# Performance work log

Measured on AMD Instinct MI355X. Metric: run time of the kernel, lower is better.

Reference implementation:

```python
import jax, jax.numpy as jnp
import numpy as np

B, T, A, IN = 128, 512, 2, 192
N_SESS, RDIM, OUT = 512, 64, 256


def setup_inputs() -> dict:
    key = jax.random.key(0)
    k1, k2, k3, k4 = jax.random.split(key, 4)
    state_in = jax.random.normal(k1, (B, T, A, IN), dtype=jnp.float32)
    session = jax.random.randint(k2, (B,), 0, N_SESS, dtype=jnp.int64)
    # kaiming-uniform-like init scale, exact distribution irrelevant for correctness baseline
    unique_readin = jax.random.normal(k3, (N_SESS, IN, RDIM), dtype=jnp.float32) * (1.0 / np.sqrt(IN))
    project = jax.random.normal(k4, (RDIM, OUT), dtype=jnp.float32) * (1.0 / np.sqrt(RDIM))
    return {"state_in": state_in, "session": session,
            "unique_readin": unique_readin, "project": project}


def reference(state_in, session, unique_readin, project):
    # gather per-sample readin matrices: [B, IN, RDIM]
    readin_matrix = unique_readin[session]
    # btai,bih->btah : per-sample matmul over the input-feature axis
    h = jnp.einsum('btai,bih->btah', state_in, readin_matrix)
    # low-rank compression projection to model dim: [B, T, A, OUT]
    out = jnp.matmul(h, project)
    return out
```

## Files before the change

### kernel.cpp

```cpp
#include <hip/hip_runtime.h>
#include <hip/hip_bf16.h>
#include <stdint.h>


typedef short    bf16x8 __attribute__((ext_vector_type(8)));
typedef float    f32x4  __attribute__((ext_vector_type(4)));
typedef uint32_t u32x2  __attribute__((ext_vector_type(2)));
typedef uint32_t u32x4  __attribute__((ext_vector_type(4)));

#define NB    128
#define MPB   1024
#define INF   192
#define RDIM  64
#define OUTF  256

#define WAIT_VM4()   asm volatile("s_waitcnt vmcnt(4)" ::: "memory")
#define WAIT_VM0()   asm volatile("s_waitcnt vmcnt(0)" ::: "memory")
#define WAIT_LGKM0() asm volatile("s_waitcnt lgkmcnt(0)" ::: "memory")

__device__ __forceinline__ uint16_t f2bf(float f) {
    union { float f; uint32_t u; } v; v.f = f;
    return (uint16_t)((v.u + 0x7fffu + ((v.u >> 16) & 1u)) >> 16);
}
__device__ __forceinline__ uint32_t pack2(float a, float b) {
    return (uint32_t)f2bf(a) | ((uint32_t)f2bf(b) << 16);
}
__device__ __forceinline__ bf16x8 cvt8(f32x4 a, f32x4 b) {
    union { __hip_bfloat162 h2[4]; bf16x8 h; } r;
    r.h2[0] = __float22bfloat162_rn({a[0], a[1]});
    r.h2[1] = __float22bfloat162_rn({a[2], a[3]});
    r.h2[2] = __float22bfloat162_rn({b[0], b[1]});
    r.h2[3] = __float22bfloat162_rn({b[2], b[3]});
    return r.h;
}
__device__ __forceinline__ void gl_lds16(const void* g, void* l) {
    auto gp = (const __attribute__((address_space(1))) uint32_t*)(uintptr_t)g;
    auto lp = (__attribute__((address_space(3))) uint32_t*)(uintptr_t)l;
    __builtin_amdgcn_global_load_lds(gp, lp, 16, 0, 0);
}

__global__ __launch_bounds__(256, 2) void fused_gemm(
    const float* __restrict__ X,
    const int*   __restrict__ session,
    const float* __restrict__ readin,
    const float* __restrict__ project,
    float*       __restrict__ Y)
{
    __shared__ __attribute__((aligned(16))) uint8_t arena[81920];

    const int bid0 = blockIdx.x;
    const int bid  = ((bid0 & 7) << 7) | (bid0 >> 3);
    const int b  = bid >> 3;
    const int mt = (bid >> 1) & 3;
    const int nt = bid & 1;
    const int t  = threadIdx.x, l = t & 63, w = t >> 6;
    const int lr = l & 15, lk = l >> 4;

    const float* Xb = X + ((size_t)b * MPB + mt * 256) * INF;
    float*       Yb = Y + ((size_t)b * MPB + mt * 256) * OUTF + nt * 128;

    uint8_t* Ab = arena + 49152 + w * 8192;
    int asrc[4];
#pragma unroll
    for (int c = 0; c < 4; ++c) {
        int i   = c * 64 + l;
        int row = i >> 3;
        int kq  = (i & 7) ^ (row & 7);
        asrc[c] = row * INF + kq * 4;
    }
    const float* Aw = Xb + (size_t)(w * 32) * INF;

    auto stage = [&](int s, int buf) {
        const float* src = Aw + (s / 6) * (128 * INF) + (s % 6) * 32;
#pragma unroll
        for (int c = 0; c < 4; ++c)
            gl_lds16(src + asrc[c], Ab + buf * 4096 + c * 1024);
    };

    stage(0, 0);
    stage(1, 1);

    {
        uint16_t* Rl = (uint16_t*)arena;
        uint16_t* Pl = (uint16_t*)(arena + 24576);
        const float* Rg = readin + (size_t)session[b] * (INF * RDIM);

#pragma unroll
        for (int c = 0; c < 3; ++c) {
            int idx = c * 4096 + t * 16;
            int row = idx >> 6;
            int kg0 = (idx & 63) >> 3;
            f32x4 v0 = *(const f32x4*)(Rg + idx);
            f32x4 v1 = *(const f32x4*)(Rg + idx + 4);
            f32x4 v2 = *(const f32x4*)(Rg + idx + 8);
            f32x4 v3 = *(const f32x4*)(Rg + idx + 12);
            u32x4 d0, d1;
            d0[0] = pack2(v0[0], v0[1]); d0[1] = pack2(v0[2], v0[3]);
            d0[2] = pack2(v1[0], v1[1]); d0[3] = pack2(v1[2], v1[3]);
            d1[0] = pack2(v2[0], v2[1]); d1[1] = pack2(v2[2], v2[3]);
            d1[2] = pack2(v3[0], v3[1]); d1[3] = pack2(v3[2], v3[3]);
            *(u32x4*)&Rl[row * 64 + (((kg0    ) ^ (row & 7)) << 3)] = d0;
            *(u32x4*)&Rl[row * 64 + (((kg0 + 1) ^ (row & 7)) << 3)] = d1;
        }
        {
            int h  = t >> 2;
            int og = (t & 3) * 32;
            const float* Pg = project + (size_t)h * OUTF + nt * 128 + og;
#pragma unroll
            for (int q = 0; q < 8; ++q) {
                f32x4 v = *(const f32x4*)(Pg + q * 4);
#pragma unroll
                for (int e = 0; e < 4; ++e) {
                    int o = og + q * 4 + e;
                    Pl[o * 64 + (((h >> 3) ^ (o & 7)) << 3) + (h & 7)] = f2bf(v[e]);
                }
            }
        }
        __syncthreads();

        const int wm = w >> 1, wn = w & 1;
        f32x4 wacc[6][4];
#pragma unroll
        for (int n = 0; n < 6; ++n)
#pragma unroll
            for (int m = 0; m < 4; ++m) wacc[n][m] = f32x4{0.f, 0.f, 0.f, 0.f};

#pragma unroll
        for (int kk = 0; kk < 2; ++kk) {
            int kg = kk * 4 + lk;
            bf16x8 a[4], bb[6];
#pragma unroll
            for (int m = 0; m < 4; ++m) {
                int row = wm * 64 + m * 16 + lr;
                a[m] = *(const bf16x8*)&Pl[row * 64 + ((kg ^ (row & 7)) << 3)];
            }
#pragma unroll
            for (int n = 0; n < 6; ++n) {
                int col = wn * 96 + n * 16 + lr;
                bb[n] = *(const bf16x8*)&Rl[col * 64 + ((kg ^ (col & 7)) << 3)];
            }
#pragma unroll
            for (int n = 0; n < 6; ++n)
#pragma unroll
                for (int m = 0; m < 4; ++m)
                    wacc[n][m] = __builtin_amdgcn_mfma_f32_16x16x32_bf16(
                        bb[n], a[m], wacc[n][m], 0, 0, 0);
        }
        __syncthreads();

        uint16_t* Bs16 = (uint16_t*)arena;
#pragma unroll
        for (int n = 0; n < 6; ++n) {
            int ubase = (wn * 12 + n * 2 + (lk >> 1)) * 128;
#pragma unroll
            for (int m = 0; m < 4; ++m) {
                int o = wm * 64 + m * 16 + lr;
                u32x2 d;
                d[0] = pack2(wacc[n][m][0], wacc[n][m][1]);
                d[1] = pack2(wacc[n][m][2], wacc[n][m][3]);
                *(u32x2*)&Bs16[(size_t)(ubase + o) * 8 + (lk & 1) * 4] = d;
            }
        }
        __syncthreads();
    }

    f32x4 accA[2][8], accB[2][8];
#pragma unroll
    for (int m = 0; m < 2; ++m)
#pragma unroll
        for (int n = 0; n < 8; ++n) {
            accA[m][n] = f32x4{0.f, 0.f, 0.f, 0.f};
            accB[m][n] = f32x4{0.f, 0.f, 0.f, 0.f};
        }

    const int a0s = ((2 * lk)     ^ (lr & 7)) << 4;
    const int a1s = ((2 * lk + 1) ^ (lr & 7)) << 4;

#pragma unroll
    for (int s = 0; s < 12; ++s) {
        if (s < 10) { WAIT_VM4(); } else { WAIT_VM0(); }
        __builtin_amdgcn_sched_barrier(0);

        const uint8_t* Abuf = Ab + (s & 1) * 4096;
        const int kk = s % 6;
        bf16x8 af[2], bfr[8];
#pragma unroll
        for (int m = 0; m < 2; ++m) {
            const uint8_t* p = Abuf + (m * 16 + lr) * 128;
            f32x4 lo = *(const f32x4*)(p + a0s);
            f32x4 hi = *(const f32x4*)(p + a1s);
            af[m] = cvt8(lo, hi);
        }
#pragma unroll
        for (int n = 0; n < 8; ++n)
            bfr[n] = *(const bf16x8*)(arena
                        + (((kk * 4 + lk) * 128 + n * 16 + lr) << 4));

        WAIT_LGKM0();
        __builtin_amdgcn_sched_barrier(0);
        if (s < 10) stage(s + 2, s & 1);

        if (s < 6) {
#pragma unroll
            for (int m = 0; m < 2; ++m)
#pragma unroll
                for (int n = 0; n < 8; ++n)
                    accA[m][n] = __builtin_amdgcn_mfma_f32_16x16x32_bf16(
                        af[m], bfr[n], accA[m][n], 0, 0, 0);
        } else {
#pragma unroll
            for (int m = 0; m < 2; ++m)
#pragma unroll
                for (int n = 0; n < 8; ++n)
                    accB[m][n] = __builtin_amdgcn_mfma_f32_16x16x32_bf16(
                        af[m], bfr[n], accB[m][n], 0, 0, 0);
        }
    }

#pragma unroll
    for (int m = 0; m < 2; ++m) {
        int r0 = w * 32 + m * 16 + lk * 4;
#pragma unroll
        for (int n = 0; n < 8; ++n) {
            int c0 = n * 16 + lr;
#pragma unroll
            for (int j = 0; j < 4; ++j) {
                Yb[(size_t)(r0 + j) * OUTF + c0]       = accA[m][n][j];
                Yb[(size_t)(128 + r0 + j) * OUTF + c0] = accB[m][n][j];
            }
        }
    }
}

extern "C" void kernel_launch(void* const* d_in, const int* in_sizes, int n_in,
                              void* d_out, int out_size, void* d_ws, size_t ws_size,
                              hipStream_t stream) {
    (void)in_sizes; (void)n_in; (void)out_size; (void)d_ws; (void)ws_size;
    const float* state   = (const float*)d_in[0];
    const int*   session = (const int*)  d_in[1];
    const float* readin  = (const float*)d_in[2];
    const float* project = (const float*)d_in[3];
    float*       out     = (float*)d_out;

    hipLaunchKernelGGL(fused_gemm, dim3(1024), dim3(256), 0, stream,
                       state, session, readin, project, out);
}
```

Baseline: 45.33 us.

## Double rows per block and stream output stores per 128-row chunk

Each block now covers 512 rows instead of 256, and the grid shrinks to 512 blocks, so the per-sample fused weight matrix (readin times project, built in bf16) is computed half as often. A single accumulator set is reused across four 128-row chunks. Each chunk's result is written as vectorized f32x4 stores inside the K loop, using swapped MFMA operands so each lane's values are contiguous along the output row. Wait counts are relaxed to let those stores overlap later loads. The risk is lower occupancy and parallelism (512 blocks over the device's CUs) and a more fragile vmcnt accounting.

```diff
diff --git a/kernel.cpp b/kernel.cpp
--- a/kernel.cpp
+++ b/kernel.cpp
@@ -14,6 +14,7 @@
 #define RDIM  64
 #define OUTF  256
 
+#define WAIT_VM20()  asm volatile("s_waitcnt vmcnt(20)" ::: "memory")
 #define WAIT_VM4()   asm volatile("s_waitcnt vmcnt(4)" ::: "memory")
 #define WAIT_VM0()   asm volatile("s_waitcnt vmcnt(0)" ::: "memory")
 #define WAIT_LGKM0() asm volatile("s_waitcnt lgkmcnt(0)" ::: "memory")
@@ -49,15 +50,15 @@
     __shared__ __attribute__((aligned(16))) uint8_t arena[81920];
 
     const int bid0 = blockIdx.x;
-    const int bid  = ((bid0 & 7) << 7) | (bid0 >> 3);
-    const int b  = bid >> 3;
-    const int mt = (bid >> 1) & 3;
+    const int bid  = ((bid0 & 7) << 6) | (bid0 >> 3);
+    const int b  = bid >> 2;
+    const int mt = (bid >> 1) & 1;
     const int nt = bid & 1;
     const int t  = threadIdx.x, l = t & 63, w = t >> 6;
     const int lr = l & 15, lk = l >> 4;
 
-    const float* Xb = X + ((size_t)b * MPB + mt * 256) * INF;
-    float*       Yb = Y + ((size_t)b * MPB + mt * 256) * OUTF + nt * 128;
+    const float* Xb = X + ((size_t)b * MPB + mt * 512) * INF;
+    float*       Yb = Y + ((size_t)b * MPB + mt * 512) * OUTF + nt * 128;
 
     uint8_t* Ab = arena + 49152 + w * 8192;
     int asrc[4];
@@ -164,25 +165,26 @@
         __syncthreads();
     }
 
-    f32x4 accA[2][8], accB[2][8];
+    f32x4 acc[2][8];
 #pragma unroll
     for (int m = 0; m < 2; ++m)
 #pragma unroll
-        for (int n = 0; n < 8; ++n) {
-            accA[m][n] = f32x4{0.f, 0.f, 0.f, 0.f};
-            accB[m][n] = f32x4{0.f, 0.f, 0.f, 0.f};
-        }
+        for (int n = 0; n < 8; ++n) acc[m][n] = f32x4{0.f, 0.f, 0.f, 0.f};
 
     const int a0s = ((2 * lk)     ^ (lr & 7)) << 4;
     const int a1s = ((2 * lk + 1) ^ (lr & 7)) << 4;
 
 #pragma unroll
-    for (int s = 0; s < 12; ++s) {
-        if (s < 10) { WAIT_VM4(); } else { WAIT_VM0(); }
+    for (int s = 0; s < 24; ++s) {
+        const int h  = s / 6;
+        const int kk = s % 6;
+
+        if (s == 23)                    { WAIT_VM0(); }
+        else if (s >= 6 && kk < 2)      { WAIT_VM20(); }
+        else                            { WAIT_VM4(); }
         __builtin_amdgcn_sched_barrier(0);
 
         const uint8_t* Abuf = Ab + (s & 1) * 4096;
-        const int kk = s % 6;
         bf16x8 af[2], bfr[8];
 #pragma unroll
         for (int m = 0; m < 2; ++m) {
@@ -198,35 +200,30 @@
 
         WAIT_LGKM0();
         __builtin_amdgcn_sched_barrier(0);
-        if (s < 10) stage(s + 2, s & 1);
-
-        if (s < 6) {
-#pragma unroll
-            for (int m = 0; m < 2; ++m)
+        if (s < 22) stage(s + 2, s & 1);
+
+#pragma unroll
+        for (int m = 0; m < 2; ++m)
+#pragma unroll
+            for (int n = 0; n < 8; ++n)
+                acc[m][n] = __builtin_amdgcn_mfma_f32_16x16x32_bf16(
+                    bfr[n], af[m], acc[m][n], 0, 0, 0);
+
+        if (kk == 5) {
+#pragma unroll
+            for (int m = 0; m < 2; ++m) {
+                float* yr = Yb + (size_t)(h * 128 + w * 32 + m * 16 + lr) * OUTF
+                          + lk * 4;
 #pragma unroll
                 for (int n = 0; n < 8; ++n)
-                    accA[m][n] = __builtin_amdgcn_mfma_f32_16x16x32_bf16(
-                        af[m], bfr[n], accA[m][n], 0, 0, 0);
-        } else {
-#pragma unroll
-            for (int m = 0; m < 2; ++m)
-#pragma unroll
-                for (int n = 0; n < 8; ++n)
-                    accB[m][n] = __builtin_amdgcn_mfma_f32_16x16x32_bf16(
-                        af[m], bfr[n], accB[m][n], 0, 0, 0);
-        }
-    }
-
-#pragma unroll
-    for (int m = 0; m < 2; ++m) {
-        int r0 = w * 32 + m * 16 + lk * 4;
-#pragma unroll
-        for (int n = 0; n < 8; ++n) {
-            int c0 = n * 16 + lr;
-#pragma unroll
-            for (int j = 0; j < 4; ++j) {
-                Yb[(size_t)(r0 + j) * OUTF + c0]       = accA[m][n][j];
-                Yb[(size_t)(128 + r0 + j) * OUTF + c0] = accB[m][n][j];
+                    *(f32x4*)(yr + n * 16) = acc[m][n];
+            }
+            if (s != 23) {
+#pragma unroll
+                for (int m = 0; m < 2; ++m)
+#pragma unroll
+                    for (int n = 0; n < 8; ++n)
+                        acc[m][n] = f32x4{0.f, 0.f, 0.f, 0.f};
             }
         }
     }
@@ -242,6 +239,6 @@
     const float* project = (const float*)d_in[3];
     float*       out     = (float*)d_out;
 
-    hipLaunchKernelGGL(fused_gemm, dim3(1024), dim3(256), 0, stream,
+    hipLaunchKernelGGL(fused_gemm, dim3(512), dim3(256), 0, stream,
                        state, session, readin, project, out);
 }
```

After: 47.24 us. +4.2%, slower.

## Use 512-thread blocks, halve per-wave tile, and store outputs mid-loop with swapped MFMA operands

Applied to the files above, without the earlier changes.

Doubles the threads per block to eight waves, so each wave handles 16 rows instead of 32. This halves the per-wave A staging, the readin/project conversion work and the weight-fusion MFMA tile. The main loop swaps the MFMA operand order so each lane holds four contiguous output columns. It writes results as 16-byte vector stores right after each half finishes, instead of scalar stores at the end, and adjusts the vmcnt waits for the overlapping store traffic. This aims to cut register pressure and uncoalesced scalar stores and to raise latency hiding, at the risk of lower occupancy with 512-thread blocks and the 80 KB LDS arena.

```diff
diff --git a/kernel.cpp b/kernel.cpp
--- a/kernel.cpp
+++ b/kernel.cpp
@@ -14,7 +14,8 @@
 #define RDIM  64
 #define OUTF  256
 
-#define WAIT_VM4()   asm volatile("s_waitcnt vmcnt(4)" ::: "memory")
+#define WAIT_VM10()  asm volatile("s_waitcnt vmcnt(10)" ::: "memory")
+#define WAIT_VM2()   asm volatile("s_waitcnt vmcnt(2)" ::: "memory")
 #define WAIT_VM0()   asm volatile("s_waitcnt vmcnt(0)" ::: "memory")
 #define WAIT_LGKM0() asm volatile("s_waitcnt lgkmcnt(0)" ::: "memory")
 
@@ -39,7 +40,7 @@
     __builtin_amdgcn_global_load_lds(gp, lp, 16, 0, 0);
 }
 
-__global__ __launch_bounds__(256, 2) void fused_gemm(
+__global__ __launch_bounds__(512, 2) void fused_gemm(
     const float* __restrict__ X,
     const int*   __restrict__ session,
     const float* __restrict__ readin,
@@ -59,22 +60,22 @@
     const float* Xb = X + ((size_t)b * MPB + mt * 256) * INF;
     float*       Yb = Y + ((size_t)b * MPB + mt * 256) * OUTF + nt * 128;
 
-    uint8_t* Ab = arena + 49152 + w * 8192;
-    int asrc[4];
-#pragma unroll
-    for (int c = 0; c < 4; ++c) {
+    uint8_t* Ab = arena + 49152 + w * 4096;
+    int asrc[2];
+#pragma unroll
+    for (int c = 0; c < 2; ++c) {
         int i   = c * 64 + l;
         int row = i >> 3;
         int kq  = (i & 7) ^ (row & 7);
         asrc[c] = row * INF + kq * 4;
     }
-    const float* Aw = Xb + (size_t)(w * 32) * INF;
+    const float* Aw = Xb + (size_t)(w * 16) * INF;
 
     auto stage = [&](int s, int buf) {
         const float* src = Aw + (s / 6) * (128 * INF) + (s % 6) * 32;
 #pragma unroll
-        for (int c = 0; c < 4; ++c)
-            gl_lds16(src + asrc[c], Ab + buf * 4096 + c * 1024);
+        for (int c = 0; c < 2; ++c)
+            gl_lds16(src + asrc[c], Ab + buf * 2048 + c * 1024);
     };
 
     stage(0, 0);
@@ -87,27 +88,22 @@
 
 #pragma unroll
         for (int c = 0; c < 3; ++c) {
-            int idx = c * 4096 + t * 16;
+            int idx = c * 4096 + t * 8;
             int row = idx >> 6;
-            int kg0 = (idx & 63) >> 3;
+            int kg0 = t & 7;
             f32x4 v0 = *(const f32x4*)(Rg + idx);
             f32x4 v1 = *(const f32x4*)(Rg + idx + 4);
-            f32x4 v2 = *(const f32x4*)(Rg + idx + 8);
-            f32x4 v3 = *(const f32x4*)(Rg + idx + 12);
-            u32x4 d0, d1;
+            u32x4 d0;
             d0[0] = pack2(v0[0], v0[1]); d0[1] = pack2(v0[2], v0[3]);
             d0[2] = pack2(v1[0], v1[1]); d0[3] = pack2(v1[2], v1[3]);
-            d1[0] = pack2(v2[0], v2[1]); d1[1] = pack2(v2[2], v2[3]);
-            d1[2] = pack2(v3[0], v3[1]); d1[3] = pack2(v3[2], v3[3]);
-            *(u32x4*)&Rl[row * 64 + (((kg0    ) ^ (row & 7)) << 3)] = d0;
-            *(u32x4*)&Rl[row * 64 + (((kg0 + 1) ^ (row & 7)) << 3)] = d1;
+            *(u32x4*)&Rl[row * 64 + ((kg0 ^ (row & 7)) << 3)] = d0;
         }
         {
-            int h  = t >> 2;
-            int og = (t & 3) * 32;
+            int h  = t >> 3;
+            int og = (t & 7) * 16;
             const float* Pg = project + (size_t)h * OUTF + nt * 128 + og;
 #pragma unroll
-            for (int q = 0; q < 8; ++q) {
+            for (int q = 0; q < 4; ++q) {
                 f32x4 v = *(const f32x4*)(Pg + q * 4);
 #pragma unroll
                 for (int e = 0; e < 4; ++e) {
@@ -118,29 +114,29 @@
         }
         __syncthreads();
 
-        const int wm = w >> 1, wn = w & 1;
-        f32x4 wacc[6][4];
-#pragma unroll
-        for (int n = 0; n < 6; ++n)
+        const int wn = w & 3, wm = w >> 2;
+        f32x4 wacc[3][4];
+#pragma unroll
+        for (int n = 0; n < 3; ++n)
 #pragma unroll
             for (int m = 0; m < 4; ++m) wacc[n][m] = f32x4{0.f, 0.f, 0.f, 0.f};
 
 #pragma unroll
         for (int kk = 0; kk < 2; ++kk) {
             int kg = kk * 4 + lk;
-            bf16x8 a[4], bb[6];
+            bf16x8 a[4], bb[3];
 #pragma unroll
             for (int m = 0; m < 4; ++m) {
                 int row = wm * 64 + m * 16 + lr;
                 a[m] = *(const bf16x8*)&Pl[row * 64 + ((kg ^ (row & 7)) << 3)];
             }
 #pragma unroll
-            for (int n = 0; n < 6; ++n) {
-                int col = wn * 96 + n * 16 + lr;
+            for (int n = 0; n < 3; ++n) {
+                int col = wn * 48 + n * 16 + lr;
                 bb[n] = *(const bf16x8*)&Rl[col * 64 + ((kg ^ (col & 7)) << 3)];
             }
 #pragma unroll
-            for (int n = 0; n < 6; ++n)
+            for (int n = 0; n < 3; ++n)
 #pragma unroll
                 for (int m = 0; m < 4; ++m)
                     wacc[n][m] = __builtin_amdgcn_mfma_f32_16x16x32_bf16(
@@ -150,8 +146,8 @@
 
         uint16_t* Bs16 = (uint16_t*)arena;
 #pragma unroll
-        for (int n = 0; n < 6; ++n) {
-            int ubase = (wn * 12 + n * 2 + (lk >> 1)) * 128;
+        for (int n = 0; n < 3; ++n) {
+            int ubase = (wn * 6 + n * 2 + (lk >> 1)) * 128;
 #pragma unroll
             for (int m = 0; m < 4; ++m) {
                 int o = wm * 64 + m * 16 + lr;
@@ -164,32 +160,30 @@
         __syncthreads();
     }
 
-    f32x4 accA[2][8], accB[2][8];
-#pragma unroll
-    for (int m = 0; m < 2; ++m)
-#pragma unroll
-        for (int n = 0; n < 8; ++n) {
-            accA[m][n] = f32x4{0.f, 0.f, 0.f, 0.f};
-            accB[m][n] = f32x4{0.f, 0.f, 0.f, 0.f};
-        }
+    f32x4 acc[8];
+#pragma unroll
+    for (int n = 0; n < 8; ++n) acc[n] = f32x4{0.f, 0.f, 0.f, 0.f};
 
     const int a0s = ((2 * lk)     ^ (lr & 7)) << 4;
     const int a1s = ((2 * lk + 1) ^ (lr & 7)) << 4;
 
 #pragma unroll
     for (int s = 0; s < 12; ++s) {
-        if (s < 10) { WAIT_VM4(); } else { WAIT_VM0(); }
+        const int h  = s / 6;
+        const int kk = s % 6;
+
+        if (s == 11)                  { WAIT_VM0(); }
+        else if (s == 6 || s == 7)    { WAIT_VM10(); }
+        else                          { WAIT_VM2(); }
         __builtin_amdgcn_sched_barrier(0);
 
-        const uint8_t* Abuf = Ab + (s & 1) * 4096;
-        const int kk = s % 6;
-        bf16x8 af[2], bfr[8];
-#pragma unroll
-        for (int m = 0; m < 2; ++m) {
-            const uint8_t* p = Abuf + (m * 16 + lr) * 128;
+        const uint8_t* Abuf = Ab + (s & 1) * 2048;
+        bf16x8 af, bfr[8];
+        {
+            const uint8_t* p = Abuf + lr * 128;
             f32x4 lo = *(const f32x4*)(p + a0s);
             f32x4 hi = *(const f32x4*)(p + a1s);
-            af[m] = cvt8(lo, hi);
+            af = cvt8(lo, hi);
         }
 #pragma unroll
         for (int n = 0; n < 8; ++n)
@@ -200,33 +194,19 @@
         __builtin_amdgcn_sched_barrier(0);
         if (s < 10) stage(s + 2, s & 1);
 
-        if (s < 6) {
-#pragma unroll
-            for (int m = 0; m < 2; ++m)
-#pragma unroll
-                for (int n = 0; n < 8; ++n)
-                    accA[m][n] = __builtin_amdgcn_mfma_f32_16x16x32_bf16(
-                        af[m], bfr[n], accA[m][n], 0, 0, 0);
-        } else {
-#pragma unroll
-            for (int m = 0; m < 2; ++m)
-#pragma unroll
-                for (int n = 0; n < 8; ++n)
-                    accB[m][n] = __builtin_amdgcn_mfma_f32_16x16x32_bf16(
-                        af[m], bfr[n], accB[m][n], 0, 0, 0);
-        }
-    }
-
-#pragma unroll
-    for (int m = 0; m < 2; ++m) {
-        int r0 = w * 32 + m * 16 + lk * 4;
-#pragma unroll
-        for (int n = 0; n < 8; ++n) {
-            int c0 = n * 16 + lr;
-#pragma unroll
-            for (int j = 0; j < 4; ++j) {
-                Yb[(size_t)(r0 + j) * OUTF + c0]       = accA[m][n][j];
-                Yb[(size_t)(128 + r0 + j) * OUTF + c0] = accB[m][n][j];
+#pragma unroll
+        for (int n = 0; n < 8; ++n)
+            acc[n] = __builtin_amdgcn_mfma_f32_16x16x32_bf16(
+                bfr[n], af, acc[n], 0, 0, 0);
+
+        if (kk == 5) {
+            float* yr = Yb + (size_t)(h * 128 + w * 16 + lr) * OUTF + lk * 4;
+#pragma unroll
+            for (int n = 0; n < 8; ++n)
+                *(f32x4*)(yr + n * 16) = acc[n];
+            if (s != 11) {
+#pragma unroll
+                for (int n = 0; n < 8; ++n) acc[n] = f32x4{0.f, 0.f, 0.f, 0.f};
             }
         }
     }
@@ -242,6 +222,6 @@
     const float* project = (const float*)d_in[3];
     float*       out     = (float*)d_out;
 
-    hipLaunchKernelGGL(fused_gemm, dim3(1024), dim3(256), 0, stream,
+    hipLaunchKernelGGL(fused_gemm, dim3(1024), dim3(512), 0, stream,
                        state, session, readin, project, out);
 }
```

Result: no change. 44.85 us, median of 2 (-1.1%).
